# Kernel tuning notes

Hardware: AMD Instinct MI355X
Metric: run time of the kernel (lower is better)

## Reference

```python
import jax, jax.numpy as jnp
import numpy as np

R = 512   # rnn_size
K = 2     # context_size (number of memories in queue)


def _lstm_cell(x, h, c, Wih, Whh, bih, bhh):
    # PyTorch LSTMCell: gates ordered i, f, g, o
    gates = x @ Wih.T + h @ Whh.T + bih + bhh
    i, f, g, o = jnp.split(gates, 4, axis=1)
    i = jax.nn.sigmoid(i)
    f = jax.nn.sigmoid(f)
    g = jnp.tanh(g)
    o = jax.nn.sigmoid(o)
    c = f * c + i * g
    h = o * jnp.tanh(c)
    return h, c


def setup_inputs() -> dict:
    key = jax.random.key(0)
    ks = jax.random.split(key, 12)
    T, B, N = 64, 16, 256
    emb_utts = jax.random.normal(ks[0], (T, B, R), jnp.float32)
    M = jax.random.normal(ks[1], (K, B, N, R), jnp.float32)
    z = jnp.zeros((B, R), jnp.float32)
    s = 0.1  # param init scale to avoid gate saturation
    params = {
        'Wih_r': s * jax.random.normal(ks[2], (4 * R, 2 * R), jnp.float32),
        'Whh_r': s * jax.random.normal(ks[3], (4 * R, R), jnp.float32),
        'bih_r': s * jax.random.normal(ks[4], (4 * R,), jnp.float32),
        'bhh_r': s * jax.random.normal(ks[5], (4 * R,), jnp.float32),
        'Wc':    s * jax.random.normal(ks[6], (R, K * R + R), jnp.float32),
        'bc':    s * jax.random.normal(ks[7], (R,), jnp.float32),
        'Wih_w': s * jax.random.normal(ks[8], (4 * R, R), jnp.float32),
        'Whh_w': s * jax.random.normal(ks[9], (4 * R, R), jnp.float32),
        'bih_w': s * jax.random.normal(ks[10], (4 * R,), jnp.float32),
        'bhh_w': s * jax.random.normal(ks[11], (4 * R,), jnp.float32),
    }
    return dict(emb_utts=emb_utts, hr0=z, cr0=z, hw0=z, cw0=z,
                init_output=z, M=M, **params)


def reference(emb_utts, hr0, cr0, hw0, cw0, init_output, M,
              Wih_r, Whh_r, bih_r, bhh_r, Wc, bc,
              Wih_w, Whh_w, bih_w, bhh_w):
    B = emb_utts.shape[1]

    def step(carry, w):
        hr, cr, hw, cw, Mq = carry
        # input_feed: out is never updated in the original loop -> init_output
        x = jnp.concatenate([w, init_output], axis=1)
        hr, cr = _lstm_cell(x, hr, cr, Wih_r, Whh_r, bih_r, bhh_r)
        # read each memory: sim [K,B,N], z softmax over slots, m [K,B,R]
        sim = jnp.einsum('br,kbnr->kbn', hr, Mq)
        z = jax.nn.softmax(sim, axis=-1)
        m = jnp.einsum('kbn,kbnr->kbr', z, Mq)
        cattet = jnp.concatenate(
            [hr, m.transpose(1, 0, 2).reshape(B, K * R)], axis=1)
        comp = jax.nn.softmax(cattet @ Wc.T + bc, axis=-1)
        hw, cw = _lstm_cell(comp, hw, cw, Wih_w, Whh_w, bih_w, bhh_w)
        # NTM-style update: M_new = (1 - z) * (M + hw)
        erase = 1.0 - z[..., None]                    # [K,B,N,1]
        Mq = erase * (Mq + hw[None, :, None, :])      # [K,B,N,R]
        return (hr, cr, hw, cw, Mq), hw

    (hr, cr, hw, cw, Mf), outputs = jax.lax.scan(
        step, (hr0, cr0, hw0, cw0, M), emb_utts)
    return outputs, hr, cr, hw, cw, Mf
```

## Files before the change

### kernel.cpp

```cpp
#include <hip/hip_runtime.h>
#include <math.h>

#define RR 512
#define BB 16
#define TT 64
#define KC 2
#define NN 256
#define NBLK 256

__device__ __forceinline__ float sigmoidf_(float x) {
    return 1.0f / (1.0f + __expf(-x));
}
__device__ __forceinline__ float wave_sum(float v) {
    #pragma unroll
    for (int off = 32; off > 0; off >>= 1) v += __shfl_xor(v, off, 64);
    return v;
}
__device__ __forceinline__ float wave_max(float v) {
    #pragma unroll
    for (int off = 32; off > 0; off >>= 1) v = fmaxf(v, __shfl_xor(v, off, 64));
    return v;
}

__device__ __forceinline__ float ldA(const float* p) {
    return __hip_atomic_load(p, __ATOMIC_RELAXED, __HIP_MEMORY_SCOPE_AGENT);
}
__device__ __forceinline__ void stA(float* p, float v) {
    __hip_atomic_store(p, v, __ATOMIC_RELAXED, __HIP_MEMORY_SCOPE_AGENT);
}
__device__ __forceinline__ unsigned ldU(const unsigned* p) {
    return __hip_atomic_load(p, __ATOMIC_RELAXED, __HIP_MEMORY_SCOPE_AGENT);
}
__device__ __forceinline__ void stU(unsigned* p, unsigned v) {
    __hip_atomic_store(p, v, __ATOMIC_RELAXED, __HIP_MEMORY_SCOPE_AGENT);
}
__device__ __forceinline__ float2 ldA2(const float* p) {
    unsigned long long v = __hip_atomic_load((const unsigned long long*)p,
                                             __ATOMIC_RELAXED, __HIP_MEMORY_SCOPE_AGENT);
    float2 r;
    r.x = __uint_as_float((unsigned)v);
    r.y = __uint_as_float((unsigned)(v >> 32));
    return r;
}
__device__ __forceinline__ void stA2(float* p, float x, float y) {
    unsigned long long v = ((unsigned long long)__float_as_uint(y) << 32)
                         | (unsigned long long)__float_as_uint(x);
    __hip_atomic_store((unsigned long long*)p, v, __ATOMIC_RELAXED,
                       __HIP_MEMORY_SCOPE_AGENT);
}

#define LDG8(d0,d1,d2,d3,d4,d5,d6,d7, q0,q1,q2,q3,q4,q5,q6,q7)      \
    asm volatile(                                                     \
        "global_load_dwordx4 %0, %8, off sc0 sc1\n\t"                \
        "global_load_dwordx4 %1, %9, off sc0 sc1\n\t"                \
        "global_load_dwordx4 %2, %10, off sc0 sc1\n\t"               \
        "global_load_dwordx4 %3, %11, off sc0 sc1\n\t"               \
        "global_load_dwordx4 %4, %12, off sc0 sc1\n\t"               \
        "global_load_dwordx4 %5, %13, off sc0 sc1\n\t"               \
        "global_load_dwordx4 %6, %14, off sc0 sc1\n\t"               \
        "global_load_dwordx4 %7, %15, off sc0 sc1\n\t"               \
        "s_waitcnt vmcnt(0)"                                          \
        : "=&v"(d0), "=&v"(d1), "=&v"(d2), "=&v"(d3),                 \
          "=&v"(d4), "=&v"(d5), "=&v"(d6), "=&v"(d7)                  \
        : "v"(q0), "v"(q1), "v"(q2), "v"(q3),                         \
          "v"(q4), "v"(q5), "v"(q6), "v"(q7)                          \
        : "memory")

#define LDG4(d0,d1,d2,d3, q0,q1,q2,q3)                                \
    asm volatile(                                                     \
        "global_load_dwordx4 %0, %4, off sc0 sc1\n\t"                \
        "global_load_dwordx4 %1, %5, off sc0 sc1\n\t"                \
        "global_load_dwordx4 %2, %6, off sc0 sc1\n\t"                \
        "global_load_dwordx4 %3, %7, off sc0 sc1\n\t"                \
        "s_waitcnt vmcnt(0)"                                          \
        : "=&v"(d0), "=&v"(d1), "=&v"(d2), "=&v"(d3)                  \
        : "v"(q0), "v"(q1), "v"(q2), "v"(q3)                          \
        : "memory")

#define LDG16O(d0,d1,d2,d3,d4,d5,d6,d7,d8,d9,d10,d11,d12,d13,d14,d15,\
               q0,q1,q2,q3)                                           \
    asm volatile(                                                     \
        "global_load_dwordx4 %0, %16, off sc0 sc1\n\t"               \
        "global_load_dwordx4 %1, %16, off offset:1024 sc0 sc1\n\t"   \
        "global_load_dwordx4 %2, %16, off offset:2048 sc0 sc1\n\t"   \
        "global_load_dwordx4 %3, %16, off offset:3072 sc0 sc1\n\t"   \
        "global_load_dwordx4 %4, %17, off sc0 sc1\n\t"               \
        "global_load_dwordx4 %5, %17, off offset:1024 sc0 sc1\n\t"   \
        "global_load_dwordx4 %6, %17, off offset:2048 sc0 sc1\n\t"   \
        "global_load_dwordx4 %7, %17, off offset:3072 sc0 sc1\n\t"   \
        "global_load_dwordx4 %8, %18, off sc0 sc1\n\t"               \
        "global_load_dwordx4 %9, %18, off offset:1024 sc0 sc1\n\t"   \
        "global_load_dwordx4 %10, %18, off offset:2048 sc0 sc1\n\t"  \
        "global_load_dwordx4 %11, %18, off offset:3072 sc0 sc1\n\t"  \
        "global_load_dwordx4 %12, %19, off sc0 sc1\n\t"              \
        "global_load_dwordx4 %13, %19, off offset:1024 sc0 sc1\n\t"  \
        "global_load_dwordx4 %14, %19, off offset:2048 sc0 sc1\n\t"  \
        "global_load_dwordx4 %15, %19, off offset:3072 sc0 sc1\n\t"  \
        "s_waitcnt vmcnt(0)"                                          \
        : "=&v"(d0), "=&v"(d1), "=&v"(d2), "=&v"(d3),                 \
          "=&v"(d4), "=&v"(d5), "=&v"(d6), "=&v"(d7),                 \
          "=&v"(d8), "=&v"(d9), "=&v"(d10), "=&v"(d11),               \
          "=&v"(d12), "=&v"(d13), "=&v"(d14), "=&v"(d15)              \
        : "v"(q0), "v"(q1), "v"(q2), "v"(q3)                          \
        : "memory")

struct f8 { float4 a, b; };
__device__ __forceinline__ f8 ld8s(const float* row, int lane) {
    f8 r;
    r.a = *(const float4*)(row + lane * 4);
    r.b = *(const float4*)(row + 256 + lane * 4);
    return r;
}
__device__ __forceinline__ void st8s(float* row, const f8& v, int lane) {
    *(float4*)(row + lane * 4) = v.a;
    *(float4*)(row + 256 + lane * 4) = v.b;
}
__device__ __forceinline__ f8 ld8sA2(const float* row, int lane) {
    float2 t0 = ldA2(row + lane * 4);
    float2 t1 = ldA2(row + lane * 4 + 2);
    float2 t2 = ldA2(row + 256 + lane * 4);
    float2 t3 = ldA2(row + 256 + lane * 4 + 2);
    f8 r;
    r.a = make_float4(t0.x, t0.y, t1.x, t1.y);
    r.b = make_float4(t2.x, t2.y, t3.x, t3.y);
    return r;
}
__device__ __forceinline__ float dot8(const f8& x, const f8& y) {
    return x.a.x*y.a.x + x.a.y*y.a.y + x.a.z*y.a.z + x.a.w*y.a.w
         + x.b.x*y.b.x + x.b.y*y.b.y + x.b.z*y.b.z + x.b.w*y.b.w;
}
__device__ __forceinline__ void upd8(f8& m, const f8& u, float zf) {
    m.a.x = zf * (m.a.x + u.a.x); m.a.y = zf * (m.a.y + u.a.y);
    m.a.z = zf * (m.a.z + u.a.z); m.a.w = zf * (m.a.w + u.a.w);
    m.b.x = zf * (m.b.x + u.b.x); m.b.y = zf * (m.b.y + u.b.y);
    m.b.z = zf * (m.b.z + u.b.z); m.b.w = zf * (m.b.w + u.b.w);
}
__device__ __forceinline__ void fmaacc8(f8& acc, float sc, const f8& m, float wgt) {
    acc.a.x = acc.a.x*sc + wgt*m.a.x; acc.a.y = acc.a.y*sc + wgt*m.a.y;
    acc.a.z = acc.a.z*sc + wgt*m.a.z; acc.a.w = acc.a.w*sc + wgt*m.a.w;
    acc.b.x = acc.b.x*sc + wgt*m.b.x; acc.b.y = acc.b.y*sc + wgt*m.b.y;
    acc.b.z = acc.b.z*sc + wgt*m.b.z; acc.b.w = acc.b.w*sc + wgt*m.b.w;
}

__device__ __forceinline__ float reduce16(float* p, int lane) {
    float q[8];
    {
        bool hi = (lane & 32) != 0;
        #pragma unroll
        for (int i = 0; i < 8; ++i) {
            float snd = hi ? p[i] : p[i + 8];
            float r = __shfl_xor(snd, 32, 64);
            q[i] = (hi ? p[i + 8] : p[i]) + r;
        }
    }
    float s4[4];
    {
        bool hi = (lane & 16) != 0;
        #pragma unroll
        for (int i = 0; i < 4; ++i) {
            float snd = hi ? q[i] : q[i + 4];
            float r = __shfl_xor(snd, 16, 64);
            s4[i] = (hi ? q[i + 4] : q[i]) + r;
        }
    }
    float d2[2];
    {
        bool hi = (lane & 8) != 0;
        #pragma unroll
        for (int i = 0; i < 2; ++i) {
            float snd = hi ? s4[i] : s4[i + 2];
            float r = __shfl_xor(snd, 8, 64);
            d2[i] = (hi ? s4[i + 2] : s4[i]) + r;
        }
    }
    float v;
    {
        bool hi = (lane & 4) != 0;
        float snd = hi ? d2[0] : d2[1];
        float r = __shfl_xor(snd, 4, 64);
        v = (hi ? d2[1] : d2[0]) + r;
    }
    v += __shfl_xor(v, 2, 64);
    v += __shfl_xor(v, 1, 64);
    return v;
}

__device__ __forceinline__ float gatedotR(const f8* A, const f8& w, int lane) {
    float p[16];
    #pragma unroll
    for (int b = 0; b < 16; ++b) p[b] = dot8(A[b], w);
    return reduce16(p, lane);
}
__device__ __forceinline__ float gatedotL(const float* act, const f8& w, int lane) {
    float p[16];
    #pragma unroll
    for (int b = 0; b < 16; ++b) {
        f8 r = ld8s(act + b * 512, lane);
        p[b] = dot8(r, w);
    }
    return reduce16(p, lane);
}
__device__ __forceinline__ void ldacts(f8* A, const float* act, int lane) {
    #pragma unroll
    for (int b = 0; b < 16; ++b) A[b] = ld8s(act + b * 512, lane);
}

__device__ __forceinline__ void barArrive(unsigned* slots, int sidx, unsigned tgt) {
    asm volatile("s_waitcnt vmcnt(0)" ::: "memory");
    __syncthreads();
    if (threadIdx.x == 0) stU(slots + sidx, tgt);
}
__device__ __forceinline__ void gridWait(unsigned* slots, unsigned tgt) {
    if (threadIdx.x < 64) {
        const unsigned* base = slots + threadIdx.x * 4;
        for (;;) {
            bool ok = (ldU(base + 0) >= tgt) & (ldU(base + 1) >= tgt)
                    & (ldU(base + 2) >= tgt) & (ldU(base + 3) >= tgt);
            if (__all(ok)) break;
            __builtin_amdgcn_s_sleep(1);
        }
    }
    __syncthreads();
}
__device__ __forceinline__ void groupWait(unsigned* slots, int gbase, unsigned tgt) {
    if (threadIdx.x < 64) {
        const unsigned* ps = slots + gbase + (threadIdx.x & 7);
        for (;;) {
            bool ok = ldU(ps) >= tgt;
            if (__all(ok)) break;
            __builtin_amdgcn_s_sleep(1);
        }
    }
    __syncthreads();
}

__global__ void k_pre(const float* __restrict__ emb, const float* __restrict__ io,
                      const float* __restrict__ Wih, const float* __restrict__ bih,
                      const float* __restrict__ bhh, float* __restrict__ pre)
{
    __shared__ float As[16][65];
    __shared__ float Bs[16][65];
    int tid = threadIdx.x;
    int row0 = blockIdx.y * 64;
    int col0 = blockIdx.x * 64;
    int ty = tid >> 4, tx = tid & 15;
    float acc[4][4] = {};
    int lr = tid >> 2;
    int lk4 = (tid & 3) * 4;
    for (int k0 = 0; k0 < 1024; k0 += 16) {
        int grow = row0 + lr;
        int b = grow & 15;
        #pragma unroll
        for (int q = 0; q < 4; ++q) {
            int k = k0 + lk4 + q;
            float v = (k < RR) ? emb[(size_t)grow * RR + k]
                               : io[(size_t)b * RR + (k - RR)];
            As[lk4 + q][lr] = v;
        }
        #pragma unroll
        for (int q = 0; q < 4; ++q) {
            int k = k0 + lk4 + q;
            Bs[lk4 + q][lr] = Wih[(size_t)(col0 + lr) * 1024 + k];
        }
        __syncthreads();
        #pragma unroll
        for (int kk = 0; kk < 16; ++kk) {
            float a[4], bbv[4];
            #pragma unroll
            for (int i = 0; i < 4; ++i) a[i] = As[kk][ty * 4 + i];
            #pragma unroll
            for (int j = 0; j < 4; ++j) bbv[j] = Bs[kk][tx * 4 + j];
            #pragma unroll
            for (int i = 0; i < 4; ++i)
                #pragma unroll
                for (int j = 0; j < 4; ++j)
                    acc[i][j] += a[i] * bbv[j];
        }
        __syncthreads();
    }
    #pragma unroll
    for (int i = 0; i < 4; ++i) {
        int grow = row0 + ty * 4 + i;
        #pragma unroll
        for (int j = 0; j < 4; ++j) {
            int gcol = col0 + tx * 4 + j;
            pre[(size_t)grow * 2048 + gcol] = acc[i][j] + bih[gcol] + bhh[gcol];
        }
    }
}

struct P {
    const float *pre, *Whh_r, *Wc, *bc, *Wih_w, *Whh_w, *bih_w, *bhh_w;
    const float *hr0, *cr0, *hw0, *cw0, *M0;
    float *mbuf, *comppre, *mpart, *mxpart, *sumpart;
    float *hrb0, *hrb1, *crS, *hwb0, *hwb1, *cwS;
    float *outputs, *Mw;
    unsigned *slots;
};

__global__ void __launch_bounds__(512, 1) k_persist(P p)
{
    const int tid = threadIdx.x;
    const int bid = blockIdx.x;
    const int wv = tid >> 6;
    const int lane = tid & 63;
    const int u0 = bid * 2;
    const int kb = (bid & 7) * 4 + (bid >> 6);
    const int w2 = (bid >> 3) & 7;
    const int bM = kb & 15;
    const int rowG = kb * 256 + w2 * 32;
    const int sidx = kb * 8 + w2;
    const int gbase = kb * 8;

    const int gateW = wv >> 1, uuW = wv & 1;
    const int jAw = gateW * 512 + u0 + uuW;

    __shared__ float Mlds[32][512];
    __shared__ float bufH[16 * 512];
    __shared__ float bufW[16 * 512];
    __shared__ float smacc[8][512];
    __shared__ float smx8[8], ssh8[8];
    __shared__ float simL[32];
    __shared__ float gsm[2][4][16];
    __shared__ float cc[2][3][16];
    __shared__ float wmx[16][2], wsm[16][2];
    __shared__ float bcsh[2];

    unsigned tg = 0;
    float mxK = 0.f, sumInvK = 0.f;
    float crR = 0.f, cwR = 0.f;

    const f8 wRj = ld8s(p.Whh_r + (size_t)jAw * 512, lane);
    const f8 wWj = ld8s(p.Whh_w + (size_t)jAw * 512, lane);
    const f8 wIj = ld8s(p.Wih_w + (size_t)jAw * 512, lane);
    const float bwj = p.bih_w[jAw] + p.bhh_w[jAw];
    const int jjC = (wv < 2) ? wv : ((wv < 4) ? wv - 2 : wv - 4);
    const int itmC = (wv < 2) ? 0 : ((wv < 4) ? 1 : 2);
    f8 wCj = {};
    if (wv < 6)
        wCj = ld8s(p.Wc + (size_t)(u0 + jjC) * 1536 + itmC * 512, lane);
    if (tid < 2) bcsh[tid] = p.bc[u0 + tid];
    if (tid < 32) cwR = p.cw0[(tid & 15) * 512 + u0 + (tid >> 4)];

    {
        const float4* src = (const float4*)(p.M0 + (size_t)rowG * 512);
        float4* dst = (float4*)&Mlds[0][0];
        #pragma unroll 2
        for (int idx = tid; idx < 32 * 128; idx += 512)
            dst[idx] = src[idx];
    }

    {
        f8 A[16]; ldacts(A, p.hr0, lane);
        float gv = gatedotR(A, wRj, lane);
        if ((lane & 3) == 0) {
            int b = (lane >> 2) & 15;
            gsm[uuW][gateW][b] = gv + p.pre[(size_t)b * 2048 + jAw];
        }
        __syncthreads();
        if (tid < 32) {
            int b = tid & 15, uu = tid >> 4;
            int u = u0 + uu;
            float gi = sigmoidf_(gsm[uu][0][b]);
            float gf = sigmoidf_(gsm[uu][1][b]);
            float gg = tanhf(gsm[uu][2][b]);
            float go = sigmoidf_(gsm[uu][3][b]);
            float c = gf * p.cr0[b * 512 + u] + gi * gg;
            crR = c;
            stA(p.hrb0 + b * 512 + u, go * tanhf(c));
        }
        ++tg; barArrive(p.slots, sidx, tg); gridWait(p.slots, tg);
    }

    for (int t = 0; t < TT; ++t) {
        const float* hrcur  = (t & 1) ? p.hrb1 : p.hrb0;
        float*       hrnext = (t & 1) ? p.hrb0 : p.hrb1;
        const float* hwprev = (t == 0) ? p.hw0 : (((t - 1) & 1) ? p.hwb1 : p.hwb0);
        float*       hwnext = (t & 1) ? p.hwb1 : p.hwb0;

        {
            float4 st[8];
            const float* h0 = hrcur + tid * 4;
            const float* g0 = hwprev + tid * 4;
            LDG8(st[0], st[1], st[2], st[3], st[4], st[5], st[6], st[7],
                 h0, h0 + 2048, h0 + 4096, h0 + 6144,
                 g0, g0 + 2048, g0 + 4096, g0 + 6144);
            #pragma unroll
            for (int q = 0; q < 4; ++q) {
                ((float4*)bufH)[q * 512 + tid] = st[q];
                ((float4*)bufW)[q * 512 + tid] = st[4 + q];
            }
        }
        __syncthreads();

        {
            f8 h = ld8s(bufH + bM * 512, lane);
            f8 w8 = {};
            if (t > 0) w8 = ld8s(bufW + bM * 512, lane);
            float mx = -3.0e38f, ssum = 0.f;
            f8 macc = {};
            #pragma unroll
            for (int ii = 0; ii < 4; ++ii) {
                int rl = wv * 4 + ii;
                float4* mp0 = (float4*)&Mlds[rl][lane * 4];
                float4* mp1 = (float4*)&Mlds[rl][256 + lane * 4];
                f8 m; m.a = *mp0; m.b = *mp1;
                if (t > 0) {
                    float zf = 1.0f - __expf(simL[rl] - mxK) * sumInvK;
                    upd8(m, w8, zf);
                    *mp0 = m.a; *mp1 = m.b;
                }
                float s = wave_sum(dot8(m, h));
                float nmx = fmaxf(mx, s);
                float sc = __expf(mx - nmx);
                float wgt = __expf(s - nmx);
                fmaacc8(macc, sc, m, wgt);
                ssum = ssum * sc + wgt;
                mx = nmx;
                if (lane == 0) simL[rl] = s;
            }
            if (lane == 0) { smx8[wv] = mx; ssh8[wv] = ssum; }
            __syncthreads();
            float MXb = smx8[0];
            #pragma unroll
            for (int w3 = 1; w3 < 8; ++w3) MXb = fmaxf(MXb, smx8[w3]);
            float sc2 = __expf(mx - MXb);
            float* d0 = &smacc[wv][lane * 4];
            float* d1 = &smacc[wv][256 + lane * 4];
            d0[0] = macc.a.x * sc2; d0[1] = macc.a.y * sc2;
            d0[2] = macc.a.z * sc2; d0[3] = macc.a.w * sc2;
            d1[0] = macc.b.x * sc2; d1[1] = macc.b.y * sc2;
            d1[2] = macc.b.z * sc2; d1[3] = macc.b.w * sc2;
            __syncthreads();
            if (tid < 256) {
                int r2 = tid * 2;
                float s0 = 0.f, s1 = 0.f;
                #pragma unroll
                for (int w3 = 0; w3 < 8; ++w3) {
                    s0 += smacc[w3][r2];
                    s1 += smacc[w3][r2 + 1];
                }
                stA2(&p.mpart[(size_t)(kb * 8 + w2) * 512 + r2], s0, s1);
            }
            if (tid == 0) {
                float sB = 0.f;
                #pragma unroll
                for (int w3 = 0; w3 < 8; ++w3)
                    sB += ssh8[w3] * __expf(smx8[w3] - MXb);
                stA(&p.mxpart[kb * 8 + w2], MXb);
                stA(&p.sumpart[kb * 8 + w2], sB);
            }
        }
        if (t < 63) {
            float gv = gatedotL(bufH, wRj, lane);
            if ((lane & 3) == 0) {
                int b = (lane >> 2) & 15;
                gsm[uuW][gateW][b] = gv + p.pre[(size_t)((t + 1) * 16 + b) * 2048 + jAw];
            }
            __syncthreads();
            if (tid < 32) {
                int b = tid & 15, uu = tid >> 4;
                int u = u0 + uu;
                float gi = sigmoidf_(gsm[uu][0][b]);
                float gf = sigmoidf_(gsm[uu][1][b]);
                float gg = tanhf(gsm[uu][2][b]);
                float go = sigmoidf_(gsm[uu][3][b]);
                float c = gf * crR + gi * gg;
                crR = c;
                stA(hrnext + b * 512 + u, go * tanhf(c));
            }
        }

        ++tg; barArrive(p.slots, sidx, tg); groupWait(p.slots, gbase, tg);
        {
            float mxp[8];
            #pragma unroll
            for (int w3 = 0; w3 < 8; ++w3) mxp[w3] = ldA(&p.mxpart[kb * 8 + w3]);
            float MX = -3.0e38f;
            #pragma unroll
            for (int w3 = 0; w3 < 8; ++w3) MX = fmaxf(MX, mxp[w3]);
            float SUM = 0.f;
            #pragma unroll
            for (int w3 = 0; w3 < 8; ++w3)
                SUM += ldA(&p.sumpart[kb * 8 + w3]) * __expf(mxp[w3] - MX);
            mxK = MX;
            sumInvK = 1.0f / SUM;
            if (tid < 32) {
                int r2 = w2 * 64 + tid * 2;
                float a0 = 0.f, a1 = 0.f;
                #pragma unroll
                for (int w3 = 0; w3 < 8; ++w3) {
                    float cf = __expf(mxp[w3] - MX);
                    float2 v2 = ldA2(&p.mpart[(size_t)(kb * 8 + w3) * 512 + r2]);
                    a0 += cf * v2.x;
                    a1 += cf * v2.y;
                }
                stA2(&p.mbuf[(size_t)kb * 512 + r2], a0 * sumInvK, a1 * sumInvK);
            }
        }
        ++tg; barArrive(p.slots, sidx, tg); gridWait(p.slots, tg);

        float vhJ = gatedotL(bufW, wWj, lane);
        {
            if (wv < 2) {
                float v = gatedotL(bufH, wCj, lane);
                if ((lane & 3) == 0) cc[jjC][0][(lane >> 2) & 15] = v;
            } else if (wv < 6) {
                f8 Am[16];
                const float* msbase = p.mbuf + (itmC - 1) * 16 * 512 + lane * 4;
                LDG16O(Am[0].a, Am[0].b, Am[1].a, Am[1].b,
                       Am[2].a, Am[2].b, Am[3].a, Am[3].b,
                       Am[4].a, Am[4].b, Am[5].a, Am[5].b,
                       Am[6].a, Am[6].b, Am[7].a, Am[7].b,
                       msbase, msbase + 1024, msbase + 2048, msbase + 3072);
                LDG16O(Am[8].a, Am[8].b, Am[9].a, Am[9].b,
                       Am[10].a, Am[10].b, Am[11].a, Am[11].b,
                       Am[12].a, Am[12].b, Am[13].a, Am[13].b,
                       Am[14].a, Am[14].b, Am[15].a, Am[15].b,
                       msbase + 4096, msbase + 5120, msbase + 6144, msbase + 7168);
                float v = gatedotR(Am, wCj, lane);
                if ((lane & 3) == 0) cc[jjC][itmC][(lane >> 2) & 15] = v;
            }
            __syncthreads();
            if (tid < 32) {
                int b = tid & 15, jj2 = tid >> 4;
                stA(&p.comppre[b * 512 + (u0 + jj2)],
                    cc[jj2][0][b] + cc[jj2][1][b] + cc[jj2][2][b] + bcsh[jj2]);
            }
        }
        ++tg; barArrive(p.slots, sidx, tg); gridWait(p.slots, tg);

        {
            float4 v4[4];
            const float* cs = p.comppre + tid * 4;
            LDG4(v4[0], v4[1], v4[2], v4[3],
                 cs, cs + 2048, cs + 4096, cs + 6144);
            const int bhalf = wv & 1, brow = wv >> 1;
            #pragma unroll
            for (int k = 0; k < 4; ++k) {
                float mk = fmaxf(fmaxf(v4[k].x, v4[k].y), fmaxf(v4[k].z, v4[k].w));
                mk = wave_max(mk);
                if (lane == 0) wmx[k * 4 + brow][bhalf] = mk;
            }
            __syncthreads();
            float4* Eld4 = (float4*)bufH;
            #pragma unroll
            for (int k = 0; k < 4; ++k) {
                int b = k * 4 + brow;
                float mxb = fmaxf(wmx[b][0], wmx[b][1]);
                float e0 = __expf(v4[k].x - mxb), e1 = __expf(v4[k].y - mxb);
                float e2 = __expf(v4[k].z - mxb), e3 = __expf(v4[k].w - mxb);
                Eld4[k * 512 + tid] = make_float4(e0, e1, e2, e3);
                float sv = wave_sum(e0 + e1 + e2 + e3);
                if (lane == 0) wsm[b][bhalf] = sv;
            }
            __syncthreads();
            float ti = gatedotL(bufH, wIj, lane);
            if ((lane & 3) == 0) {
                int bb = (lane >> 2) & 15;
                float siv = 1.0f / (wsm[bb][0] + wsm[bb][1]);
                gsm[uuW][gateW][bb] = ti * siv + vhJ + bwj;
            }
            __syncthreads();
            if (tid < 32) {
                int bb = tid & 15, uu = tid >> 4;
                int u = u0 + uu;
                float gi = sigmoidf_(gsm[uu][0][bb]);
                float gf = sigmoidf_(gsm[uu][1][bb]);
                float gg = tanhf(gsm[uu][2][bb]);
                float go = sigmoidf_(gsm[uu][3][bb]);
                float c = gf * cwR + gi * gg;
                cwR = c;
                float h = go * tanhf(c);
                stA(hwnext + bb * 512 + u, h);
                p.outputs[(size_t)t * 8192 + bb * 512 + u] = h;
            }
        }
        ++tg; barArrive(p.slots, sidx, tg); gridWait(p.slots, tg);
    }

    {
        f8 w8 = ld8sA2(p.hwb1 + (size_t)bM * 512, lane);
        #pragma unroll
        for (int ii = 0; ii < 4; ++ii) {
            int rl = wv * 4 + ii;
            float zf = 1.0f - __expf(simL[rl] - mxK) * sumInvK;
            f8 m;
            m.a = *(float4*)&Mlds[rl][lane * 4];
            m.b = *(float4*)&Mlds[rl][256 + lane * 4];
            upd8(m, w8, zf);
            st8s(p.Mw + (size_t)(rowG + rl) * 512, m, lane);
        }
        if (tid < 32) {
            int b = tid & 15, uu = tid >> 4;
            int u = u0 + uu;
            p.crS[b * 512 + u] = crR;
            p.cwS[b * 512 + u] = cwR;
        }
    }
}

extern "C" void kernel_launch(void* const* d_in, const int* in_sizes, int n_in,
                              void* d_out, int out_size, void* d_ws, size_t ws_size,
                              hipStream_t stream) {
    const float* emb   = (const float*)d_in[0];
    const float* hr0   = (const float*)d_in[1];
    const float* cr0   = (const float*)d_in[2];
    const float* hw0   = (const float*)d_in[3];
    const float* cw0   = (const float*)d_in[4];
    const float* io    = (const float*)d_in[5];
    const float* M0    = (const float*)d_in[6];
    const float* Wih_r = (const float*)d_in[7];
    const float* bih_r = (const float*)d_in[9];
    const float* bhh_r = (const float*)d_in[10];

    float* out = (float*)d_out;
    float* outputs = out;
    float* hrS1 = out + 524288;
    float* crS  = out + 532480;
    float* hwS1 = out + 540672;
    float* cwS  = out + 548864;
    float* Mw   = out + 557056;

    float* ws = (float*)d_ws;
    float* pre     = ws;
    float* mbuf    = ws + 2097152;
    float* comppre = mbuf + 16384;
    float* hrB0    = comppre + 8192;
    float* hwB0    = hrB0 + 8192;
    float* mpart   = hwB0 + 8192;
    float* mxpart  = mpart + 131072;
    float* sumpart = mxpart + 256;
    unsigned* slots = (unsigned*)(sumpart + 256);

    (void)hipMemsetAsync(slots, 0, 256 * sizeof(unsigned), stream);

    k_pre<<<dim3(32, 16), 256, 0, stream>>>(emb, io, Wih_r, bih_r, bhh_r, pre);

    P p;
    p.pre = pre;
    p.Whh_r = (const float*)d_in[8];
    p.Wc    = (const float*)d_in[11];
    p.bc    = (const float*)d_in[12];
    p.Wih_w = (const float*)d_in[13];
    p.Whh_w = (const float*)d_in[14];
    p.bih_w = (const float*)d_in[15];
    p.bhh_w = (const float*)d_in[16];
    p.hr0 = hr0; p.cr0 = cr0; p.hw0 = hw0; p.cw0 = cw0; p.M0 = M0;
    p.mbuf = mbuf; p.comppre = comppre;
    p.mpart = mpart; p.mxpart = mxpart; p.sumpart = sumpart;
    p.hrb0 = hrB0; p.hrb1 = hrS1; p.crS = crS;
    p.hwb0 = hwB0; p.hwb1 = hwS1; p.cwS = cwS;
    p.outputs = outputs; p.Mw = Mw;
    p.slots = slots;

    k_persist<<<NBLK, 512, 0, stream>>>(p);
}
```

Measured before the change: 1.646 ms.

## Precompute next-step memory similarity dot products in idle waves

Uses the identity (1-z)*(M+hw)·h = (1-z)*(M·h + hw·h) to avoid recomputing full dot products after the memory update. Idle waves 6-7 compute M·h_next for the next step's hidden state during the composition phase and store the results in shared memory. The main loop then needs only one hw·h dot per block instead of 32 row dots. This relies on the next hidden state being available at that point, and it changes the floating-point summation order.

Result: faster. 1.593 ms (-3.3%).

```diff
diff --git a/kernel.cpp b/kernel.cpp
--- a/kernel.cpp
+++ b/kernel.cpp
@@ -75,6 +75,15 @@
         "s_waitcnt vmcnt(0)"                                          \
         : "=&v"(d0), "=&v"(d1), "=&v"(d2), "=&v"(d3)                  \
         : "v"(q0), "v"(q1), "v"(q2), "v"(q3)                          \
+        : "memory")
+
+#define LDG2(d0,d1, q0,q1)                                            \
+    asm volatile(                                                     \
+        "global_load_dwordx4 %0, %2, off sc0 sc1\n\t"                \
+        "global_load_dwordx4 %1, %3, off sc0 sc1\n\t"                \
+        "s_waitcnt vmcnt(0)"                                          \
+        : "=&v"(d0), "=&v"(d1)                                        \
+        : "v"(q0), "v"(q1)                                            \
         : "memory")
 
 #define LDG16O(d0,d1,d2,d3,d4,d5,d6,d7,d8,d9,d10,d11,d12,d13,d14,d15,\
@@ -321,6 +330,7 @@
     __shared__ float smacc[8][512];
     __shared__ float smx8[8], ssh8[8];
     __shared__ float simL[32];
+    __shared__ float dotN[32];
     __shared__ float gsm[2][4][16];
     __shared__ float cc[2][3][16];
     __shared__ float wmx[16][2], wsm[16][2];
@@ -396,7 +406,11 @@
         {
             f8 h = ld8s(bufH + bM * 512, lane);
             f8 w8 = {};
-            if (t > 0) w8 = ld8s(bufW + bM * 512, lane);
+            float hwDot = 0.f;
+            if (t > 0) {
+                w8 = ld8s(bufW + bM * 512, lane);
+                hwDot = wave_sum(dot8(w8, h));
+            }
             float mx = -3.0e38f, ssum = 0.f;
             f8 macc = {};
             #pragma unroll
@@ -405,12 +419,15 @@
                 float4* mp0 = (float4*)&Mlds[rl][lane * 4];
                 float4* mp1 = (float4*)&Mlds[rl][256 + lane * 4];
                 f8 m; m.a = *mp0; m.b = *mp1;
+                float s;
                 if (t > 0) {
                     float zf = 1.0f - __expf(simL[rl] - mxK) * sumInvK;
                     upd8(m, w8, zf);
                     *mp0 = m.a; *mp1 = m.b;
+                    s = zf * (dotN[rl] + hwDot);
+                } else {
+                    s = wave_sum(dot8(m, h));
                 }
-                float s = wave_sum(dot8(m, h));
                 float nmx = fmaxf(mx, s);
                 float sc = __expf(mx - nmx);
                 float wgt = __expf(s - nmx);
@@ -520,6 +537,17 @@
                        msbase + 4096, msbase + 5120, msbase + 6144, msbase + 7168);
                 float v = gatedotR(Am, wCj, lane);
                 if ((lane & 3) == 0) cc[jjC][itmC][(lane >> 2) & 15] = v;
+            } else if (t < 63) {
+                f8 hN;
+                const float* hp = hrnext + bM * 512;
+                LDG2(hN.a, hN.b, hp + lane * 4, hp + 256 + lane * 4);
+                float pp[16];
+                int rbase = (wv - 6) * 16;
+                #pragma unroll
+                for (int r = 0; r < 16; ++r)
+                    pp[r] = dot8(ld8s(&Mlds[rbase + r][0], lane), hN);
+                float v = reduce16(pp, lane);
+                if ((lane & 3) == 0) dotN[rbase + ((lane >> 2) & 15)] = v;
             }
             __syncthreads();
             if (tid < 32) {
```
